# Optimization experiments

Hardware: AMD Instinct MI355X
Metric: run time of the kernel (lower is better)

## Reference

```python
import jax, jax.numpy as jnp
import numpy as np

K = 3  # hardcoded in TransitionUp.forward

def setup_inputs() -> dict:
    key = jax.random.key(0)
    ks = jax.random.split(key, 8)
    M, N = 32768, 8192
    UP_C, DOWN_C, OUT_C = 128, 256, 128
    return {
        "up_points": jax.random.normal(ks[0], (M, 3), dtype=jnp.float32),
        "up_features": jax.random.normal(ks[1], (M, UP_C), dtype=jnp.float32),
        "down_points": jax.random.normal(ks[2], (N, 3), dtype=jnp.float32),
        "down_features": jax.random.normal(ks[3], (N, DOWN_C), dtype=jnp.float32),
        # torch nn.Linear params: W [out,in], b [out]
        "W_up": jax.random.normal(ks[4], (OUT_C, UP_C), dtype=jnp.float32) / np.sqrt(UP_C),
        "b_up": jax.random.normal(ks[5], (OUT_C,), dtype=jnp.float32) * 0.01,
        "W_down": jax.random.normal(ks[6], (OUT_C, DOWN_C), dtype=jnp.float32) / np.sqrt(DOWN_C),
        "b_down": jax.random.normal(ks[7], (OUT_C,), dtype=jnp.float32) * 0.01,
    }

def interpolate_knn(query_points, dataset_points, dataset_features, k):
    # squared pairwise distances [M, N]
    delta = query_points[:, None, :] - dataset_points[None, :, :]
    dist = jnp.sum(delta * delta, axis=-1)
    neg_dist, knn_idx = jax.lax.top_k(-dist, k)  # smallest-k
    knn_dist = -neg_dist                           # [M, k]
    knn_feats = dataset_features[knn_idx]          # [M, k, C]
    recip = 1.0 / (knn_dist + 1e-8)
    weights = recip / jnp.sum(recip, axis=-1, keepdims=True)  # [M, k]
    return jnp.einsum('mk,mkc->mc', weights, knn_feats)

def reference(up_points, up_features, down_points, down_features, W_up, b_up, W_down, b_down):
    down_f = down_features @ W_down.T + b_down            # [N, OUT_C]
    interp_f = interpolate_knn(up_points, down_points, down_f, K)  # [M, OUT_C]
    return interp_f + (up_features @ W_up.T + b_up)
```

## Files before the change

### kernel.cpp

```cpp
#include <hip/hip_runtime.h>
#include <cfloat>

#define M_UP   32768
#define N_DOWN 8192
#define UPC    128
#define DOWNC  256
#define OUTC   128
#define NCHUNK 8
#define CHUNK  (N_DOWN / NCHUNK)
#define G      8
#define Q      2
#define PG     12

__device__ __forceinline__ void fma4(float4& acc, float s, const float4 w) {
    acc.x = fmaf(s, w.x, acc.x);
    acc.y = fmaf(s, w.y, acc.y);
    acc.z = fmaf(s, w.z, acc.z);
    acc.w = fmaf(s, w.w, acc.w);
}

__device__ __forceinline__ void top3_bl(float s, int idx,
                                        float& d0, float& d1, float& d2,
                                        int& i0, int& i1, int& i2) {
    bool c0 = s < d0, c1 = s < d1, c2 = s < d2;
    float n0 = fminf(d0, s);
    float n1 = __builtin_amdgcn_fmed3f(d0, d1, s);
    float n2 = __builtin_amdgcn_fmed3f(d1, d2, s);
    int m0 = c0 ? idx : i0;
    int m1 = c0 ? i0 : (c1 ? idx : i1);
    int m2 = c1 ? i1 : (c2 ? idx : i2);
    d0 = n0; d1 = n1; d2 = n2;
    i0 = m0; i1 = m1; i2 = m2;
}

__global__ __launch_bounds__(256) void transpose_w(
        const float* __restrict__ W_up, const float* __restrict__ W_down,
        float* __restrict__ wt_up, float* __restrict__ wt_down) {
    int e = blockIdx.x * 256 + threadIdx.x;
    if (e < DOWNC * OUTC) {
        int k = e >> 7, c = e & 127;
        wt_down[e] = W_down[c * DOWNC + k];
    } else {
        int e2 = e - DOWNC * OUTC;
        int k = e2 >> 7, c = e2 & 127;
        wt_up[e2] = W_up[c * UPC + k];
    }
}

template <int K>
__device__ __forceinline__ void gemm_tile32(
        const float* __restrict__ A, const float* __restrict__ WT,
        float* sA , float* sW ,
        int rbase, int tid, float4 acc[2][2]) {
    const int rl = tid & 15;
    const int c0 = (tid >> 4) * 8;
    #pragma unroll 1
    for (int ph = 0; ph < K / 32; ++ph) {
        if (ph) __syncthreads();
        {
            int r = tid >> 3, k4 = tid & 7;
            float4 v = *(const float4*)(A + (size_t)(rbase + r) * K + ph * 32 + k4 * 4);
            *(float4*)&sA[r * 36 + k4 * 4] = v;
        }
        #pragma unroll
        for (int i = 0; i < 4; ++i) {
            int idx = tid + i * 256;
            int kk = idx >> 5, cc = idx & 31;
            float4 v = *(const float4*)(WT + (size_t)(ph * 32 + kk) * OUTC + cc * 4);
            *(float4*)&sW[kk * OUTC + cc * 4] = v;
        }
        __syncthreads();
        #pragma unroll 4
        for (int kk = 0; kk < 32; ++kk) {
            float a0 = sA[rl * 36 + kk];
            float a1 = sA[(rl + 16) * 36 + kk];
            float4 w0 = *(const float4*)&sW[kk * OUTC + c0];
            float4 w1 = *(const float4*)&sW[kk * OUTC + c0 + 4];
            fma4(acc[0][0], a0, w0); fma4(acc[0][1], a0, w1);
            fma4(acc[1][0], a1, w0); fma4(acc[1][1], a1, w1);
        }
    }
}

__device__ __forceinline__ void down_body(
        const float* __restrict__ A, const float* __restrict__ WT,
        const float* __restrict__ bias, float* __restrict__ down_f,
        int rb, int tid, float* smem) {
    float* sA = smem;
    float* sW = smem + 1152;
    float4 acc[2][2] = {};
    gemm_tile32<DOWNC>(A, WT, sA, sW, rb * 32, tid, acc);
    const int rl = tid & 15;
    const int cg = (tid >> 4) * 2;
    const float4 b0 = ((const float4*)bias)[cg];
    const float4 b1 = ((const float4*)bias)[cg + 1];
    #pragma unroll
    for (int i = 0; i < 2; ++i) {
        const int row = rb * 32 + rl + 16 * i;
        float4 v0 = acc[i][0], v1 = acc[i][1];
        v0.x += b0.x; v0.y += b0.y; v0.z += b0.z; v0.w += b0.w;
        v1.x += b1.x; v1.y += b1.y; v1.z += b1.z; v1.w += b1.w;
        ((float4*)down_f)[row * 32 + cg] = v0;
        ((float4*)down_f)[row * 32 + cg + 1] = v1;
    }
}

__device__ __forceinline__ void knn_body(
        const float* __restrict__ up_points,
        const float* __restrict__ down_points,
        float2* __restrict__ part,
        int bx, int by, int tid, float* smem) {
    float* sx = smem;
    float* sy = smem + 1536;
    float* sz = smem + 3072;
    const int base = by * CHUNK;
    for (int t = tid; t < CHUNK; t += 256) {
        int g = base + t;
        int gi = t >> 3, j = t & 7;
        sx[PG * gi + j] = down_points[3 * g];
        sy[PG * gi + j] = down_points[3 * g + 1];
        sz[PG * gi + j] = down_points[3 * g + 2];
    }
    __syncthreads();

    const int m0 = bx * (256 * Q) + tid;
    const int m1 = m0 + 256;
    const float q0x = up_points[3 * m0];
    const float q0y = up_points[3 * m0 + 1];
    const float q0z = up_points[3 * m0 + 2];
    const float q1x = up_points[3 * m1];
    const float q1y = up_points[3 * m1 + 1];
    const float q1z = up_points[3 * m1 + 2];

    float a_gd0 = FLT_MAX, a_gd1 = FLT_MAX, a_gd2 = FLT_MAX;
    int   a_gi0 = 0, a_gi1 = 0, a_gi2 = 0;
    float b_gd0 = FLT_MAX, b_gd1 = FLT_MAX, b_gd2 = FLT_MAX;
    int   b_gi0 = 0, b_gi1 = 0, b_gi2 = 0;

    for (int gi = 0; gi < CHUNK / G; ++gi) {
        float4 x0 = *(const float4*)&sx[PG * gi], x1 = *(const float4*)&sx[PG * gi + 4];
        float4 y0 = *(const float4*)&sy[PG * gi], y1 = *(const float4*)&sy[PG * gi + 4];
        float4 z0 = *(const float4*)&sz[PG * gi], z1 = *(const float4*)&sz[PG * gi + 4];
        float px[G] = {x0.x, x0.y, x0.z, x0.w, x1.x, x1.y, x1.z, x1.w};
        float py[G] = {y0.x, y0.y, y0.z, y0.w, y1.x, y1.y, y1.z, y1.w};
        float pz[G] = {z0.x, z0.y, z0.z, z0.w, z1.x, z1.y, z1.z, z1.w};
        float s0[G], s1[G];
        #pragma unroll
        for (int j = 0; j < G; ++j) {
            float dx0 = q0x - px[j], dy0 = q0y - py[j], dz0 = q0z - pz[j];
            s0[j] = fmaf(dz0, dz0, fmaf(dy0, dy0, dx0 * dx0));
            float dx1 = q1x - px[j], dy1 = q1y - py[j], dz1 = q1z - pz[j];
            s1[j] = fmaf(dz1, dz1, fmaf(dy1, dy1, dx1 * dx1));
        }
        float gm0 = fminf(fminf(fminf(s0[0], s0[1]), fminf(s0[2], s0[3])),
                          fminf(fminf(s0[4], s0[5]), fminf(s0[6], s0[7])));
        float gm1 = fminf(fminf(fminf(s1[0], s1[1]), fminf(s1[2], s1[3])),
                          fminf(fminf(s1[4], s1[5]), fminf(s1[6], s1[7])));
        top3_bl(gm0, gi, a_gd0, a_gd1, a_gd2, a_gi0, a_gi1, a_gi2);
        top3_bl(gm1, gi, b_gd0, b_gd1, b_gd2, b_gi0, b_gi1, b_gi2);
    }

    #pragma unroll
    for (int qq = 0; qq < Q; ++qq) {
        const float qx = qq ? q1x : q0x;
        const float qy = qq ? q1y : q0y;
        const float qz = qq ? q1z : q0z;
        int bases[3];
        if (qq == 0) { bases[0] = a_gi0; bases[1] = a_gi1; bases[2] = a_gi2; }
        else         { bases[0] = b_gi0; bases[1] = b_gi1; bases[2] = b_gi2; }
        float D0 = FLT_MAX, D1 = FLT_MAX, D2 = FLT_MAX;
        int I0 = 0, I1 = 0, I2 = 0;
        #pragma unroll
        for (int t = 0; t < 3; ++t) {
            const int gb = bases[t];
            float4 x0 = *(const float4*)&sx[PG * gb], x1 = *(const float4*)&sx[PG * gb + 4];
            float4 y0 = *(const float4*)&sy[PG * gb], y1 = *(const float4*)&sy[PG * gb + 4];
            float4 z0 = *(const float4*)&sz[PG * gb], z1 = *(const float4*)&sz[PG * gb + 4];
            float px[G] = {x0.x, x0.y, x0.z, x0.w, x1.x, x1.y, x1.z, x1.w};
            float py[G] = {y0.x, y0.y, y0.z, y0.w, y1.x, y1.y, y1.z, y1.w};
            float pz[G] = {z0.x, z0.y, z0.z, z0.w, z1.x, z1.y, z1.z, z1.w};
            #pragma unroll
            for (int j = 0; j < G; ++j) {
                float dx = qx - px[j], dy = qy - py[j], dz = qz - pz[j];
                float s = fmaf(dz, dz, fmaf(dy, dy, dx * dx));
                top3_bl(s, base + gb * G + j, D0, D1, D2, I0, I1, I2);
            }
        }
        const int m = qq ? m1 : m0;
        const int o = (by * M_UP + m) * 3;
        part[o]     = make_float2(D0, __int_as_float(I0));
        part[o + 1] = make_float2(D1, __int_as_float(I1));
        part[o + 2] = make_float2(D2, __int_as_float(I2));
    }
}

__global__ __launch_bounds__(256) void fused_dp_knn(
        const float* __restrict__ down_features, const float* __restrict__ wt_down,
        const float* __restrict__ b_down, float* __restrict__ down_f,
        const float* __restrict__ up_points, const float* __restrict__ down_points,
        float2* __restrict__ part) {
    __shared__ __align__(16) float smem[5248];
    const int bid = blockIdx.x;
    if (bid < 512) {
        knn_body(up_points, down_points, part, bid & 63, bid >> 6,
                 threadIdx.x, smem);
    } else {
        down_body(down_features, wt_down, b_down, down_f, bid - 512,
                  threadIdx.x, smem);
    }
}

__global__ __launch_bounds__(256) void up_fused(
        const float* __restrict__ A, const float* __restrict__ WT,
        const float* __restrict__ bias, const float* __restrict__ down_f,
        const float2* __restrict__ part,
        float* __restrict__ out) {
    __shared__ __align__(16) float sA[32 * 36];
    __shared__ __align__(16) float sW[32 * OUTC];
    float4 acc[2][2] = {};
    gemm_tile32<UPC>(A, WT, sA, sW, blockIdx.x * 32, threadIdx.x, acc);

    const int rl = threadIdx.x & 15;
    const int cg = (threadIdx.x >> 4) * 2;
    const float4 b0 = ((const float4*)bias)[cg];
    const float4 b1 = ((const float4*)bias)[cg + 1];
    const float4* df4 = (const float4*)down_f;
    #pragma unroll
    for (int i = 0; i < 2; ++i) {
        const int m = blockIdx.x * 32 + rl + 16 * i;
        float D0 = FLT_MAX, D1 = FLT_MAX, D2 = FLT_MAX;
        int I0 = 0, I1 = 0, I2 = 0;
        #pragma unroll
        for (int s = 0; s < NCHUNK; ++s) {
            const float2* p = part + ((size_t)s * M_UP + m) * 3;
            #pragma unroll
            for (int j = 0; j < 3; ++j) {
                float2 v = p[j];
                top3_bl(v.x, __float_as_int(v.y), D0, D1, D2, I0, I1, I2);
            }
        }
        float r0 = 1.f / (D0 + 1e-8f);
        float r1 = 1.f / (D1 + 1e-8f);
        float r2 = 1.f / (D2 + 1e-8f);
        float rs = (r0 + r1) + r2;
        float w0 = r0 / rs, w1 = r1 / rs, w2 = r2 / rs;
        float4 f00 = df4[I0 * 32 + cg],     f01 = df4[I0 * 32 + cg + 1];
        float4 f10 = df4[I1 * 32 + cg],     f11 = df4[I1 * 32 + cg + 1];
        float4 f20 = df4[I2 * 32 + cg],     f21 = df4[I2 * 32 + cg + 1];
        float4 v0 = acc[i][0], v1 = acc[i][1];
        float4 res0, res1;
        res0.x = v0.x + b0.x + fmaf(w0, f00.x, fmaf(w1, f10.x, w2 * f20.x));
        res0.y = v0.y + b0.y + fmaf(w0, f00.y, fmaf(w1, f10.y, w2 * f20.y));
        res0.z = v0.z + b0.z + fmaf(w0, f00.z, fmaf(w1, f10.z, w2 * f20.z));
        res0.w = v0.w + b0.w + fmaf(w0, f00.w, fmaf(w1, f10.w, w2 * f20.w));
        res1.x = v1.x + b1.x + fmaf(w0, f01.x, fmaf(w1, f11.x, w2 * f21.x));
        res1.y = v1.y + b1.y + fmaf(w0, f01.y, fmaf(w1, f11.y, w2 * f21.y));
        res1.z = v1.z + b1.z + fmaf(w0, f01.z, fmaf(w1, f11.z, w2 * f21.z));
        res1.w = v1.w + b1.w + fmaf(w0, f01.w, fmaf(w1, f11.w, w2 * f21.w));
        ((float4*)out)[m * 32 + cg] = res0;
        ((float4*)out)[m * 32 + cg + 1] = res1;
    }
}

extern "C" void kernel_launch(void* const* d_in, const int* in_sizes, int n_in,
                              void* d_out, int out_size, void* d_ws, size_t ws_size,
                              hipStream_t stream) {
    const float* up_points     = (const float*)d_in[0];
    const float* up_features   = (const float*)d_in[1];
    const float* down_points   = (const float*)d_in[2];
    const float* down_features = (const float*)d_in[3];
    const float* W_up          = (const float*)d_in[4];
    const float* b_up          = (const float*)d_in[5];
    const float* W_down        = (const float*)d_in[6];
    const float* b_down        = (const float*)d_in[7];
    float* out = (float*)d_out;

    float* wt_down = (float*)d_ws;
    float* wt_up   = wt_down + DOWNC * OUTC;
    float* down_f  = wt_up + UPC * OUTC;
    float2* part   = (float2*)(down_f + N_DOWN * OUTC);

    transpose_w<<<(DOWNC * OUTC + UPC * OUTC) / 256, 256, 0, stream>>>(
        W_up, W_down, wt_up, wt_down);
    fused_dp_knn<<<768, 256, 0, stream>>>(
        down_features, wt_down, b_down, down_f, up_points, down_points, part);
    up_fused<<<M_UP / 32, 256, 0, stream>>>(
        up_features, wt_up, b_up, down_f, part, out);
}
```

Before: 173.8 us.

## Enlarge up_fused GEMM tile to 64 rows with transposed A in shared memory

Replaces the 32-row gemm_tile32 helper in up_fused with an inline 64-row tile that stages A transposed in shared memory, with each thread computing a 4x8 output block. Column ownership changes so each thread covers two 64-float halves, and the grid is halved. The aim is more register reuse per shared-memory load and half as many blocks loading the W tile. In exchange it uses more registers and the epilogue's knn merge and gather run per row with less parallelism per block.

Result: faster. 167.9 us (-3.4%).

```diff
diff --git a/kernel.cpp b/kernel.cpp
--- a/kernel.cpp
+++ b/kernel.cpp
@@ -215,50 +215,84 @@
         const float* __restrict__ bias, const float* __restrict__ down_f,
         const float2* __restrict__ part,
         float* __restrict__ out) {
-    __shared__ __align__(16) float sA[32 * 36];
-    __shared__ __align__(16) float sW[32 * OUTC];
-    float4 acc[2][2] = {};
-    gemm_tile32<UPC>(A, WT, sA, sW, blockIdx.x * 32, threadIdx.x, acc);
-
-    const int rl = threadIdx.x & 15;
-    const int cg = (threadIdx.x >> 4) * 2;
-    const float4 b0 = ((const float4*)bias)[cg];
-    const float4 b1 = ((const float4*)bias)[cg + 1];
+    __shared__ __align__(16) float sAT[32][72];
+    __shared__ __align__(16) float sW[32][128];
+    const int tid = threadIdx.x;
+    const int rt4 = (tid >> 4) * 4;
+    const int ct  = tid & 15;
+    const int rbase = blockIdx.x * 64;
+
+    float4 acc[4][2] = {};
+    #pragma unroll 1
+    for (int ph = 0; ph < UPC / 32; ++ph) {
+        if (ph) __syncthreads();
+        {
+            const int r = tid & 63, kq = tid >> 6;
+            const float* Ar = A + (size_t)(rbase + r) * UPC + ph * 32 + kq * 8;
+            float4 v0 = *(const float4*)Ar;
+            float4 v1 = *(const float4*)(Ar + 4);
+            const int k0 = kq * 8;
+            sAT[k0 + 0][r] = v0.x; sAT[k0 + 1][r] = v0.y;
+            sAT[k0 + 2][r] = v0.z; sAT[k0 + 3][r] = v0.w;
+            sAT[k0 + 4][r] = v1.x; sAT[k0 + 5][r] = v1.y;
+            sAT[k0 + 6][r] = v1.z; sAT[k0 + 7][r] = v1.w;
+        }
+        {
+            const float4* Wp = (const float4*)(WT + (size_t)ph * 32 * OUTC);
+            float4* sW4 = (float4*)&sW[0][0];
+            #pragma unroll
+            for (int i = 0; i < 4; ++i)
+                sW4[tid + i * 256] = Wp[tid + i * 256];
+        }
+        __syncthreads();
+        #pragma unroll 4
+        for (int kk = 0; kk < 32; ++kk) {
+            float4 a  = *(const float4*)&sAT[kk][rt4];
+            float4 w0 = *(const float4*)&sW[kk][ct * 4];
+            float4 w1 = *(const float4*)&sW[kk][64 + ct * 4];
+            fma4(acc[0][0], a.x, w0); fma4(acc[0][1], a.x, w1);
+            fma4(acc[1][0], a.y, w0); fma4(acc[1][1], a.y, w1);
+            fma4(acc[2][0], a.z, w0); fma4(acc[2][1], a.z, w1);
+            fma4(acc[3][0], a.w, w0); fma4(acc[3][1], a.w, w1);
+        }
+    }
+
+    const float4 b0 = ((const float4*)bias)[ct];
+    const float4 b1 = ((const float4*)bias)[ct + 16];
     const float4* df4 = (const float4*)down_f;
+    float4* out4 = (float4*)out;
     #pragma unroll
-    for (int i = 0; i < 2; ++i) {
-        const int m = blockIdx.x * 32 + rl + 16 * i;
+    for (int i = 0; i < 4; ++i) {
+        const int m = rbase + rt4 + i;
         float D0 = FLT_MAX, D1 = FLT_MAX, D2 = FLT_MAX;
         int I0 = 0, I1 = 0, I2 = 0;
         #pragma unroll
         for (int s = 0; s < NCHUNK; ++s) {
             const float2* p = part + ((size_t)s * M_UP + m) * 3;
-            #pragma unroll
-            for (int j = 0; j < 3; ++j) {
-                float2 v = p[j];
-                top3_bl(v.x, __float_as_int(v.y), D0, D1, D2, I0, I1, I2);
-            }
+            float2 v0 = p[0], v1 = p[1], v2 = p[2];
+            top3_bl(v0.x, __float_as_int(v0.y), D0, D1, D2, I0, I1, I2);
+            top3_bl(v1.x, __float_as_int(v1.y), D0, D1, D2, I0, I1, I2);
+            top3_bl(v2.x, __float_as_int(v2.y), D0, D1, D2, I0, I1, I2);
         }
         float r0 = 1.f / (D0 + 1e-8f);
         float r1 = 1.f / (D1 + 1e-8f);
         float r2 = 1.f / (D2 + 1e-8f);
         float rs = (r0 + r1) + r2;
         float w0 = r0 / rs, w1 = r1 / rs, w2 = r2 / rs;
-        float4 f00 = df4[I0 * 32 + cg],     f01 = df4[I0 * 32 + cg + 1];
-        float4 f10 = df4[I1 * 32 + cg],     f11 = df4[I1 * 32 + cg + 1];
-        float4 f20 = df4[I2 * 32 + cg],     f21 = df4[I2 * 32 + cg + 1];
-        float4 v0 = acc[i][0], v1 = acc[i][1];
+        float4 f00 = df4[I0 * 32 + ct], f01 = df4[I0 * 32 + ct + 16];
+        float4 f10 = df4[I1 * 32 + ct], f11 = df4[I1 * 32 + ct + 16];
+        float4 f20 = df4[I2 * 32 + ct], f21 = df4[I2 * 32 + ct + 16];
         float4 res0, res1;
-        res0.x = v0.x + b0.x + fmaf(w0, f00.x, fmaf(w1, f10.x, w2 * f20.x));
-        res0.y = v0.y + b0.y + fmaf(w0, f00.y, fmaf(w1, f10.y, w2 * f20.y));
-        res0.z = v0.z + b0.z + fmaf(w0, f00.z, fmaf(w1, f10.z, w2 * f20.z));
-        res0.w = v0.w + b0.w + fmaf(w0, f00.w, fmaf(w1, f10.w, w2 * f20.w));
-        res1.x = v1.x + b1.x + fmaf(w0, f01.x, fmaf(w1, f11.x, w2 * f21.x));
-        res1.y = v1.y + b1.y + fmaf(w0, f01.y, fmaf(w1, f11.y, w2 * f21.y));
-        res1.z = v1.z + b1.z + fmaf(w0, f01.z, fmaf(w1, f11.z, w2 * f21.z));
-        res1.w = v1.w + b1.w + fmaf(w0, f01.w, fmaf(w1, f11.w, w2 * f21.w));
-        ((float4*)out)[m * 32 + cg] = res0;
-        ((float4*)out)[m * 32 + cg + 1] = res1;
+        res0.x = acc[i][0].x + b0.x + fmaf(w0, f00.x, fmaf(w1, f10.x, w2 * f20.x));
+        res0.y = acc[i][0].y + b0.y + fmaf(w0, f00.y, fmaf(w1, f10.y, w2 * f20.y));
+        res0.z = acc[i][0].z + b0.z + fmaf(w0, f00.z, fmaf(w1, f10.z, w2 * f20.z));
+        res0.w = acc[i][0].w + b0.w + fmaf(w0, f00.w, fmaf(w1, f10.w, w2 * f20.w));
+        res1.x = acc[i][1].x + b1.x + fmaf(w0, f01.x, fmaf(w1, f11.x, w2 * f21.x));
+        res1.y = acc[i][1].y + b1.y + fmaf(w0, f01.y, fmaf(w1, f11.y, w2 * f21.y));
+        res1.z = acc[i][1].z + b1.z + fmaf(w0, f01.z, fmaf(w1, f11.z, w2 * f21.z));
+        res1.w = acc[i][1].w + b1.w + fmaf(w0, f01.w, fmaf(w1, f11.w, w2 * f21.w));
+        out4[m * 32 + ct] = res0;
+        out4[m * 32 + ct + 16] = res1;
     }
 }
 
@@ -284,6 +318,6 @@
         W_up, W_down, wt_up, wt_down);
     fused_dp_knn<<<768, 256, 0, stream>>>(
         down_features, wt_down, b_down, down_f, up_points, down_points, part);
-    up_fused<<<M_UP / 32, 256, 0, stream>>>(
+    up_fused<<<M_UP / 64, 256, 0, stream>>>(
         up_features, wt_up, b_up, down_f, part, out);
 }
```
